# Optimization experiments

Hardware: AMD Instinct MI355X
Metric: run time of the kernel (lower is better)

The kernel has to match this reference:

```python
import jax, jax.numpy as jnp
import numpy as np
from jax import lax

N, S, F_IN = 50000, 16, 64
HID, HEADS = 128, 4
C = HID // HEADS  # 32
E = 1600000
NEG_SLOPE = 0.2


def setup_inputs() -> dict:
    key = jax.random.key(0)
    ks = jax.random.split(key, 16)
    sc = lambda *sh: 1.0 / np.sqrt(sh[-1])
    inp = {}
    inp['node_features_sequence'] = jax.random.normal(ks[0], (N, S, F_IN), dtype=jnp.float32)
    inp['edge_index'] = jax.random.randint(ks[1], (2, E), 0, N, dtype=jnp.int64)
    # GRU params (single layer, order r,z,n as in torch)
    inp['gru_w_ih'] = jax.random.normal(ks[2], (3 * HID, F_IN), jnp.float32) * sc(F_IN)
    inp['gru_w_hh'] = jax.random.normal(ks[3], (3 * HID, HID), jnp.float32) * sc(HID)
    inp['gru_b_ih'] = jax.random.normal(ks[4], (3 * HID,), jnp.float32) * 0.01
    inp['gru_b_hh'] = jax.random.normal(ks[5], (3 * HID,), jnp.float32) * 0.01
    # GAT layer 1
    inp['gat1_w'] = jax.random.normal(ks[6], (HID, HID), jnp.float32) * sc(HID)
    inp['gat1_a_src'] = jax.random.normal(ks[7], (HEADS, C), jnp.float32) * sc(C)
    inp['gat1_a_dst'] = jax.random.normal(ks[8], (HEADS, C), jnp.float32) * sc(C)
    inp['gat1_b'] = jnp.zeros((HID,), jnp.float32)
    # GAT layer 2
    inp['gat2_w'] = jax.random.normal(ks[9], (HID, HID), jnp.float32) * sc(HID)
    inp['gat2_a_src'] = jax.random.normal(ks[10], (HEADS, C), jnp.float32) * sc(C)
    inp['gat2_a_dst'] = jax.random.normal(ks[11], (HEADS, C), jnp.float32) * sc(C)
    inp['gat2_b'] = jnp.zeros((HID,), jnp.float32)
    # classifier
    inp['clf_w'] = jax.random.normal(ks[12], (1, HID), jnp.float32) * sc(HID)
    inp['clf_b'] = jnp.zeros((1,), jnp.float32)
    return inp


def gru_last(xs, w_ih, w_hh, b_ih, b_hh):
    # xs: [N, S, F] -> last hidden [N, H]
    n, _, _ = xs.shape
    h_dim = w_hh.shape[1]
    gi_all = jnp.einsum('nsf,gf->nsg', xs, w_ih) + b_ih  # [N,S,3H]
    gi_all = jnp.swapaxes(gi_all, 0, 1)  # [S,N,3H]

    def step(h, gi):
        gh = h @ w_hh.T + b_hh
        i_r, i_z, i_n = jnp.split(gi, 3, axis=-1)
        h_r, h_z, h_n = jnp.split(gh, 3, axis=-1)
        r = jax.nn.sigmoid(i_r + h_r)
        z = jax.nn.sigmoid(i_z + h_z)
        nn_ = jnp.tanh(i_n + r * h_n)
        h_new = (1.0 - z) * nn_ + z * h
        return h_new, None

    h0 = jnp.zeros((n, h_dim), xs.dtype)
    h_last, _ = lax.scan(step, h0, gi_all)
    return h_last


def gat_layer(x, src, dst, w, a_src, a_dst, b):
    # x: [N, HID]; PyG GATConv with add_self_loops, concat heads
    n = x.shape[0]
    h = (x @ w.T).reshape(n, HEADS, C)  # [N,H,C]
    a_s = jnp.einsum('nhc,hc->nh', h, a_src)  # [N,H]
    a_d = jnp.einsum('nhc,hc->nh', h, a_dst)
    e = jax.nn.leaky_relu(a_s[src] + a_d[dst], NEG_SLOPE)  # [E',H]
    m = jax.ops.segment_max(e, dst, num_segments=n)
    m = jnp.where(jnp.isfinite(m), m, 0.0)
    ex = jnp.exp(e - m[dst])
    denom = jax.ops.segment_sum(ex, dst, num_segments=n)
    alpha = ex / (denom[dst] + 1e-16)  # [E',H]
    msg = h[src] * alpha[:, :, None]  # [E',H,C]
    out = jax.ops.segment_sum(msg, dst, num_segments=n)  # [N,H,C]
    return out.reshape(n, HEADS * C) + b


def reference(node_features_sequence, edge_index,
              gru_w_ih, gru_w_hh, gru_b_ih, gru_b_hh,
              gat1_w, gat1_a_src, gat1_a_dst, gat1_b,
              gat2_w, gat2_a_src, gat2_a_dst, gat2_b,
              clf_w, clf_b):
    n = node_features_sequence.shape[0]
    # add self loops once (same structure for both layers)
    loops = jnp.arange(n, dtype=edge_index.dtype)
    src = jnp.concatenate([edge_index[0], loops])
    dst = jnp.concatenate([edge_index[1], loops])

    x = gru_last(node_features_sequence, gru_w_ih, gru_w_hh, gru_b_ih, gru_b_hh)
    x = jax.nn.elu(gat_layer(x, src, dst, gat1_w, gat1_a_src, gat1_a_dst, gat1_b))
    x = jax.nn.elu(gat_layer(x, src, dst, gat2_w, gat2_a_src, gat2_a_dst, gat2_b))
    return jax.nn.sigmoid(x @ clf_w.T + clf_b)  # [N,1]
```

## Files before the change

kernel.cpp:

```cpp
#include <hip/hip_runtime.h>
#include <hip/hip_bf16.h>
#include <hip/hip_fp16.h>
#include <math.h>

#define N_NODES 50000
#define NP      50048
#define SEQ     16
#define FIN     64
#define HID     128
#define NEDGE   1600000
#define NB_SCAN 196
#define AGG_CAP 96

typedef __attribute__((ext_vector_type(8))) short short8;
typedef __attribute__((ext_vector_type(4))) float f32x4;

__device__ __forceinline__ float lrelu02(float v) { return v > 0.f ? v : 0.2f * v; }
__device__ __forceinline__ float frcp(float v) { return __builtin_amdgcn_rcpf(v); }
__device__ __forceinline__ float ex2(float v) { return __builtin_amdgcn_exp2f(v); }
__device__ __forceinline__ float sigmoidf_(float v) { return frcp(1.f + __expf(-v)); }
__device__ __forceinline__ float eluf_(float v) { return v > 0.f ? v : (__expf(v) - 1.f); }

__device__ __forceinline__ unsigned bfpk(float lo, float hi) {
    union { __hip_bfloat162 h; unsigned u; } c;
    c.h = __float22bfloat162_rn(make_float2(lo, hi));
    return c.u;
}
__device__ __forceinline__ unsigned hfpk(float lo, float hi) {
    union { __half2 h; unsigned u; } c;
    c.h = __float22half2_rn(make_float2(lo, hi));
    return c.u;
}
__device__ __forceinline__ float2 h2f2(unsigned u) {
    union { unsigned u; __half2 h; } c;
    c.u = u;
    return __half22float2(c.h);
}
__device__ __forceinline__ short8 pack8s(float4 a, float4 b, float s) {
    union { short8 sv; unsigned u[4]; } r;
    r.u[0] = bfpk(a.x * s, a.y * s); r.u[1] = bfpk(a.z * s, a.w * s);
    r.u[2] = bfpk(b.x * s, b.y * s); r.u[3] = bfpk(b.z * s, b.w * s);
    return r.sv;
}

#define BAR() do { asm volatile("s_waitcnt lgkmcnt(0)" ::: "memory"); \
                   __builtin_amdgcn_s_barrier(); } while (0)

__global__ __launch_bounds__(512, 2) void gru_fused(
    const float* __restrict__ x,
    const float* __restrict__ w_ih,
    const float* __restrict__ w_hh,
    const float* __restrict__ b_ih,
    const float* __restrict__ b_hh,
    float* __restrict__ hout)
{
    __shared__ __align__(16) short hA[2][2][32][136];
    __shared__ __align__(16) short xB[2][2][32][72];

    const int tid  = threadIdx.x;
    const int wave = tid >> 6;
    const int lane = tid & 63;
    const int q    = lane >> 4;
    const int rl   = lane & 15;
    const int n0   = blockIdx.x * 64;
    const int ch   = wave * 16 + rl;

    const float S1 = 1.44269504088896341f;
    const float S2 = 2.88539008177792682f;
    short8 whhf[3][4];
    short8 wihf[3][2];
#pragma unroll
    for (int g = 0; g < 3; g++) {
        const float gs = (g == 2) ? S2 : S1;
        int row = g * 128 + ch;
#pragma unroll
        for (int kc = 0; kc < 4; kc++) {
            const float* p = w_hh + row * HID + kc * 32 + q * 8;
            whhf[g][kc] = pack8s(*(const float4*)p, *(const float4*)(p + 4), gs);
        }
#pragma unroll
        for (int kc = 0; kc < 2; kc++) {
            const float* p = w_ih + row * FIN + kc * 32 + q * 8;
            wihf[g][kc] = pack8s(*(const float4*)p, *(const float4*)(p + 4), gs);
        }
    }

    const float br  = (b_ih[ch] + b_hh[ch]) * S1;
    const float bz  = (b_ih[128 + ch] + b_hh[128 + ch]) * S1;
    const float bin = b_ih[256 + ch] * S2;
    const float bhn = b_hh[256 + ch] * S2;

    const int sn = tid >> 4;
    const int sk = (tid & 15) * 4;
    int g0n = n0 + sn;      if (g0n > N_NODES - 1) g0n = N_NODES - 1;
    int g1n = n0 + 32 + sn; if (g1n > N_NODES - 1) g1n = N_NODES - 1;
    const float* xs0 = x + (size_t)g0n * SEQ * FIN + sk;
    const float* xs1 = x + (size_t)g1n * SEQ * FIN + sk;

    float hreg[2][2][4];
#pragma unroll
    for (int g = 0; g < 2; g++)
#pragma unroll
        for (int mt = 0; mt < 2; mt++)
#pragma unroll
            for (int r = 0; r < 4; r++) hreg[g][mt][r] = 0.f;

    unsigned hp01[2], hp23[2];
    float4 xhold;

    {
        float4 v = *(const float4*)(xs0);
        int2 pv;
        pv.x = (int)bfpk(v.x, v.y);
        pv.y = (int)bfpk(v.z, v.w);
        *(int2*)&xB[0][0][sn][sk] = pv;
    }
    xhold = *(const float4*)(xs1);
    BAR();

#define GRU_PHASE(G, DO_HW, HWB, DO_XW, XWB, DO_XL, XLP)                          \
    {                                                                             \
        const int rb = (t - 1) & 1;                                               \
        short8 xf[2][2], hf[2][4];                                                \
        _Pragma("unroll")                                                         \
        for (int mt = 0; mt < 2; mt++)                                            \
            _Pragma("unroll")                                                     \
            for (int kc = 0; kc < 2; kc++)                                        \
                xf[mt][kc] = *(const short8*)&xB[G][t & 1][mt * 16 + rl][kc * 32 + q * 8]; \
        if (t > 0) {                                                              \
            _Pragma("unroll")                                                     \
            for (int mt = 0; mt < 2; mt++)                                        \
                _Pragma("unroll")                                                 \
                for (int kc = 0; kc < 4; kc++)                                    \
                    hf[mt][kc] = *(const short8*)&hA[G][rb][mt * 16 + rl][kc * 32 + q * 8]; \
        }                                                                         \
                         \
        if (DO_HW) {                                                              \
            _Pragma("unroll")                                                     \
            for (int mt = 0; mt < 2; mt++) {                                      \
                const int nb = mt * 16 + q * 4;                                   \
                hA[G ^ 1][HWB][nb + 0][ch] = (short)(hp01[mt] & 0xFFFF);          \
                hA[G ^ 1][HWB][nb + 1][ch] = (short)(hp01[mt] >> 16);             \
                hA[G ^ 1][HWB][nb + 2][ch] = (short)(hp23[mt] & 0xFFFF);          \
                hA[G ^ 1][HWB][nb + 3][ch] = (short)(hp23[mt] >> 16);             \
            }                                                                     \
        }                                                                         \
        if (DO_XW) {                                                              \
            int2 pv;                                                              \
            pv.x = (int)bfpk(xhold.x, xhold.y);                                   \
            pv.y = (int)bfpk(xhold.z, xhold.w);                                   \
            *(int2*)&xB[G ^ 1][XWB][sn][sk] = pv;                                 \
        }                                                                         \
        if (DO_XL) xhold = *(const float4*)(XLP);        \
        f32x4 accr[2], accz[2], accin[2], acchn[2];                               \
        _Pragma("unroll")                                                         \
        for (int mt = 0; mt < 2; mt++) {                                          \
            accr[mt] = (f32x4)0.f; accz[mt] = (f32x4)0.f;                         \
            accin[mt] = (f32x4)0.f; acchn[mt] = (f32x4)0.f;                       \
            _Pragma("unroll")                                                     \
            for (int kc = 0; kc < 2; kc++) {                                      \
                accr[mt]  = __builtin_amdgcn_mfma_f32_16x16x32_bf16(xf[mt][kc], wihf[0][kc], accr[mt], 0, 0, 0);  \
                accz[mt]  = __builtin_amdgcn_mfma_f32_16x16x32_bf16(xf[mt][kc], wihf[1][kc], accz[mt], 0, 0, 0);  \
                accin[mt] = __builtin_amdgcn_mfma_f32_16x16x32_bf16(xf[mt][kc], wihf[2][kc], accin[mt], 0, 0, 0); \
            }                                                                     \
            if (t > 0) {                                                          \
                _Pragma("unroll")                                                 \
                for (int kc = 0; kc < 4; kc++) {                                  \
                    accr[mt]  = __builtin_amdgcn_mfma_f32_16x16x32_bf16(hf[mt][kc], whhf[0][kc], accr[mt], 0, 0, 0);  \
                    accz[mt]  = __builtin_amdgcn_mfma_f32_16x16x32_bf16(hf[mt][kc], whhf[1][kc], accz[mt], 0, 0, 0);  \
                    acchn[mt] = __builtin_amdgcn_mfma_f32_16x16x32_bf16(hf[mt][kc], whhf[2][kc], acchn[mt], 0, 0, 0); \
                }                                                                 \
            }                                                                     \
        }                                                                         \
        _Pragma("unroll")                                                         \
        for (int mt = 0; mt < 2; mt++) {                                          \
            float rg[4], zg[4], et[4], hv[4];                                     \
            _Pragma("unroll")                                                     \
            for (int r = 0; r < 4; r++) {                                         \
                float er = ex2(fminf(-(accr[mt][r] + br), 60.f));                 \
                float ez = ex2(fminf(-(accz[mt][r] + bz), 60.f));                 \
                float dr = er + 1.f, dz = ez + 1.f;                               \
                float ip = frcp(dr * dz);                                         \
                rg[r] = dz * ip; zg[r] = dr * ip;                                 \
                float ap = accin[mt][r] + bin + rg[r] * (acchn[mt][r] + bhn);     \
                et[r] = ex2(fminf(ap, 120.f));                                    \
            }                                                                     \
            _Pragma("unroll")                                                     \
            for (int pr = 0; pr < 2; pr++) {                                      \
                float d0 = et[2 * pr] + 1.f, d1 = et[2 * pr + 1] + 1.f;           \
                float ipt = frcp(d0 * d1);                                        \
                float nn0 = 1.f - 2.f * (ipt * d1);                               \
                float nn1 = 1.f - 2.f * (ipt * d0);                               \
                float h0 = zg[2 * pr]     * (hreg[G][mt][2 * pr]     - nn0) + nn0; \
                float h1 = zg[2 * pr + 1] * (hreg[G][mt][2 * pr + 1] - nn1) + nn1; \
                hreg[G][mt][2 * pr] = h0; hreg[G][mt][2 * pr + 1] = h1;           \
                hv[2 * pr] = h0; hv[2 * pr + 1] = h1;                             \
            }                                                                     \
            hp01[mt] = bfpk(hv[0], hv[1]);                                        \
            hp23[mt] = bfpk(hv[2], hv[3]);                                        \
        }                                                                         \
        BAR();                                                                    \
    }

    for (int t = 0; t < SEQ; t++) {
        GRU_PHASE(0, (t > 0), ((t - 1) & 1), 1, (t & 1),
                  (t + 1 < SEQ), (xs0 + (t + 1) * FIN))
        GRU_PHASE(1, 1, (t & 1), (t + 1 < SEQ), ((t + 1) & 1),
                  (t + 1 < SEQ), (xs1 + (t + 1) * FIN))
    }
#undef GRU_PHASE

#pragma unroll
    for (int g = 0; g < 2; g++)
#pragma unroll
        for (int mt = 0; mt < 2; mt++)
#pragma unroll
            for (int r = 0; r < 4; r++)
                hout[(size_t)(n0 + g * 32 + mt * 16 + q * 4 + r) * HID + ch] = hreg[g][mt][r];
}

__global__ void prep_weights(const float* __restrict__ g1w, const float* __restrict__ g2w,
                             float* __restrict__ g1T, float* __restrict__ g2T)
{
    int i = blockIdx.x * 256 + threadIdx.x;
    if (i < 128 * 128) {
        int k = i >> 7, g = i & 127;
        g1T[i] = g1w[g * 128 + k];
        g2T[i] = g2w[g * 128 + k];
    }
}

__global__ void count_edges(const int* __restrict__ dst, int* __restrict__ deg, int e)
{
    int i = blockIdx.x * 256 + threadIdx.x;
    if (i < e) atomicAdd(&deg[dst[i]], 1);
}

__device__ __forceinline__ int block_scan_inc(int v)
{
    int tid = threadIdx.x, lane = tid & 63, w = tid >> 6;
#pragma unroll
    for (int off = 1; off < 64; off <<= 1) {
        int tmp = __shfl_up(v, off, 64);
        if (lane >= off) v += tmp;
    }
    __shared__ int wsum[4];
    if (lane == 63) wsum[w] = v;
    __syncthreads();
    int add = 0;
    for (int i = 0; i < w; i++) add += wsum[i];
    return v + add;
}

__global__ void scan_block_sums(const int* __restrict__ deg, int* __restrict__ bsum, int n)
{
    int i = blockIdx.x * 256 + threadIdx.x;
    int v = (i < n) ? deg[i] : 0;
#pragma unroll
    for (int off = 32; off >= 1; off >>= 1) v += __shfl_xor(v, off, 64);
    __shared__ int ws[4];
    if ((threadIdx.x & 63) == 0) ws[threadIdx.x >> 6] = v;
    __syncthreads();
    if (threadIdx.x == 0) bsum[blockIdx.x] = ws[0] + ws[1] + ws[2] + ws[3];
}

__global__ void scan_bsum(int* __restrict__ bsum, int nb)
{
    int tid = threadIdx.x;
    int v = (tid < nb) ? bsum[tid] : 0;
    v = block_scan_inc(v);
    if (tid < nb) bsum[tid] = v;
}

__global__ void scan_final(const int* __restrict__ deg, const int* __restrict__ bsum,
                           int* __restrict__ rp, int n)
{
    int i = blockIdx.x * 256 + threadIdx.x;
    int v = (i < n) ? deg[i] : 0;
    int s = block_scan_inc(v);
    int add = (blockIdx.x > 0) ? bsum[blockIdx.x - 1] : 0;
    if (i < n) rp[i + 1] = s + add;
    if (i == 0) rp[0] = 0;
}

__global__ void fill_edges(const int* __restrict__ src, const int* __restrict__ dst,
                           const int* __restrict__ rp, int* __restrict__ cur,
                           int* __restrict__ col, int e)
{
    int i = blockIdx.x * 256 + threadIdx.x;
    if (i < e) {
        int d = dst[i];
        int pos = atomicAdd(&cur[d], 1);
        col[rp[d] + pos] = src[i];
    }
}

__global__ __launch_bounds__(256) void proj_attn(
    const float* __restrict__ x, const float* __restrict__ wT,
    const float* __restrict__ a_src, const float* __restrict__ a_dst,
    unsigned* __restrict__ hph, float* __restrict__ as_, float* __restrict__ ad_)
{
    __shared__ float xt[32][33];
    __shared__ float wt[32][128];
    __shared__ float ot[32][132];
    const int tid = threadIdx.x;
    const int tx = tid & 7;
    const int ty = tid >> 3;
    const int n0 = blockIdx.x * 32;
    float acc[4][4];
#pragma unroll
    for (int i = 0; i < 4; i++)
#pragma unroll
        for (int j = 0; j < 4; j++) acc[i][j] = 0.f;

    for (int k0 = 0; k0 < 128; k0 += 32) {
        __syncthreads();
#pragma unroll
        for (int i = 0; i < 4; i++) {
            int flat = tid + i * 256;
            int n = flat >> 5, k = flat & 31;
            xt[n][k] = x[(n0 + n) * HID + k0 + k];
        }
#pragma unroll
        for (int i = 0; i < 16; i++) {
            int flat = tid + i * 256;
            int kk = flat >> 7, g = flat & 127;
            wt[kk][g] = wT[(k0 + kk) * HID + g];
        }
        __syncthreads();
#pragma unroll 8
        for (int kk = 0; kk < 32; kk++) {
            float xv[4];
#pragma unroll
            for (int i = 0; i < 4; i++) xv[i] = xt[tx * 4 + i][kk];
            float4 wv = *(const float4*)&wt[kk][ty * 4];
#pragma unroll
            for (int i = 0; i < 4; i++) {
                acc[i][0] = fmaf(xv[i], wv.x, acc[i][0]);
                acc[i][1] = fmaf(xv[i], wv.y, acc[i][1]);
                acc[i][2] = fmaf(xv[i], wv.z, acc[i][2]);
                acc[i][3] = fmaf(xv[i], wv.w, acc[i][3]);
            }
        }
    }
#pragma unroll
    for (int i = 0; i < 4; i++) {
        int node = tx * 4 + i;
        ot[node][ty * 4 + 0] = acc[i][0];
        ot[node][ty * 4 + 1] = acc[i][1];
        ot[node][ty * 4 + 2] = acc[i][2];
        ot[node][ty * 4 + 3] = acc[i][3];
        uint2 pv;
        pv.x = hfpk(acc[i][0], acc[i][1]);
        pv.y = hfpk(acc[i][2], acc[i][3]);
        *(uint2*)&hph[(size_t)(n0 + node) * 64 + ty * 2] = pv;
    }
    __syncthreads();
    if (tid < 128) {
        int node = tid >> 2, head = tid & 3;
        const float* ar = a_src + head * 32;
        const float* br = a_dst + head * 32;
        float s = 0.f, d = 0.f;
#pragma unroll
        for (int j = 0; j < 32; j += 4) {
            float4 hv = *(const float4*)&ot[node][head * 32 + j];
            float4 av = *(const float4*)&ar[j];
            float4 bv = *(const float4*)&br[j];
            s += hv.x * av.x + hv.y * av.y + hv.z * av.z + hv.w * av.w;
            d += hv.x * bv.x + hv.y * bv.y + hv.z * bv.z + hv.w * bv.w;
        }
        as_[(n0 + node) * 4 + head] = s;
        ad_[(n0 + node) * 4 + head] = d;
    }
}

template <bool CLF>
__global__ __launch_bounds__(256) void gat_agg(
    const unsigned* __restrict__ hph, const float* __restrict__ as_,
    const float* __restrict__ ad_, const int* __restrict__ rp,
    const int* __restrict__ col, const float* __restrict__ bias,
    float* __restrict__ out, const float* __restrict__ cw,
    const float* __restrict__ cb, int n_nodes)
{
    __shared__ float exl[4][AGG_CAP][4];
    const int widx = threadIdx.x >> 6;
    const int lane = threadIdx.x & 63;
    const int n = blockIdx.x * 4 + widx;
    if (n >= n_nodes) return;

    const int e0 = rp[n], e1 = rp[n + 1];
    const int deg = e1 - e0;
    float4 adv = *(const float4*)&ad_[n * 4];
    float4 asn = *(const float4*)&as_[n * 4];
    float xs0 = __expf(lrelu02(asn.x + adv.x)), xs1 = __expf(lrelu02(asn.y + adv.y));
    float xs2 = __expf(lrelu02(asn.z + adv.z)), xs3 = __expf(lrelu02(asn.w + adv.w));

    float d0 = 0.f, d1 = 0.f, d2 = 0.f, d3 = 0.f;
    for (int e = e0 + lane; e < e1; e += 64) {
        int s = col[e];
        float4 a = *(const float4*)&as_[s * 4];
        float x0 = __expf(lrelu02(a.x + adv.x));
        float x1 = __expf(lrelu02(a.y + adv.y));
        float x2 = __expf(lrelu02(a.z + adv.z));
        float x3 = __expf(lrelu02(a.w + adv.w));
        int idx = e - e0;
        if (idx < AGG_CAP) {
            exl[widx][idx][0] = x0; exl[widx][idx][1] = x1;
            exl[widx][idx][2] = x2; exl[widx][idx][3] = x3;
        }
        d0 += x0; d1 += x1; d2 += x2; d3 += x3;
    }
#pragma unroll
    for (int off = 32; off >= 1; off >>= 1) {
        d0 += __shfl_xor(d0, off, 64);
        d1 += __shfl_xor(d1, off, 64);
        d2 += __shfl_xor(d2, off, 64);
        d3 += __shfl_xor(d3, off, 64);
    }
    d0 += xs0; d1 += xs1; d2 += xs2; d3 += xs3;
    float i0 = frcp(d0 + 1e-16f), i1 = frcp(d1 + 1e-16f);
    float i2 = frcp(d2 + 1e-16f), i3 = frcp(d3 + 1e-16f);

    const int head = lane >> 4;
    float invh = (head == 0) ? i0 : (head == 1) ? i1 : (head == 2) ? i2 : i3;
    float exsh = (head == 0) ? xs0 : (head == 1) ? xs1 : (head == 2) ? xs2 : xs3;
    float adh  = (head == 0) ? adv.x : (head == 1) ? adv.y : (head == 2) ? adv.z : adv.w;

    float2 sv = h2f2(hph[(size_t)n * 64 + lane]);
    float acc0 = exsh * sv.x;
    float acc1 = exsh * sv.y;

    if (deg <= AGG_CAP) {
        int e = e0;
        for (; e + 4 <= e1; e += 4) {
            int s_[4]; float w_[4]; unsigned u_[4];
#pragma unroll
            for (int u = 0; u < 4; u++) {
                s_[u] = col[e + u];
                w_[u] = exl[widx][e + u - e0][head];
            }
#pragma unroll
            for (int u = 0; u < 4; u++)
                u_[u] = hph[(size_t)s_[u] * 64 + lane];
#pragma unroll
            for (int u = 0; u < 4; u++) {
                float2 f = h2f2(u_[u]);
                acc0 = fmaf(w_[u], f.x, acc0);
                acc1 = fmaf(w_[u], f.y, acc1);
            }
        }
        for (; e < e1; e++) {
            int s = col[e];
            float w = exl[widx][e - e0][head];
            float2 f = h2f2(hph[(size_t)s * 64 + lane]);
            acc0 = fmaf(w, f.x, acc0);
            acc1 = fmaf(w, f.y, acc1);
        }
    } else {
        for (int e = e0; e < e1; e++) {
            int s = col[e];
            int idx = e - e0;
            float w;
            if (idx < AGG_CAP) w = exl[widx][idx][head];
            else               w = __expf(lrelu02(as_[s * 4 + head] + adh));
            float2 f = h2f2(hph[(size_t)s * 64 + lane]);
            acc0 = fmaf(w, f.x, acc0);
            acc1 = fmaf(w, f.y, acc1);
        }
    }

    float2 b2 = *(const float2*)&bias[2 * lane];
    float o0 = eluf_(acc0 * invh + b2.x);
    float o1 = eluf_(acc1 * invh + b2.y);
    if (CLF) {
        float2 cwv = *(const float2*)&cw[2 * lane];
        float v = o0 * cwv.x + o1 * cwv.y;
#pragma unroll
        for (int off = 32; off >= 1; off >>= 1) v += __shfl_xor(v, off, 64);
        if (lane == 0) out[n] = sigmoidf_(v + cb[0]);
    } else {
        *(float2*)&out[(size_t)n * HID + 2 * lane] = make_float2(o0, o1);
    }
}

extern "C" void kernel_launch(void* const* d_in, const int* in_sizes, int n_in,
                              void* d_out, int out_size, void* d_ws, size_t ws_size,
                              hipStream_t stream)
{
    const float* x     = (const float*)d_in[0];
    const int*   ei    = (const int*)d_in[1];
    const float* w_ih  = (const float*)d_in[2];
    const float* w_hh  = (const float*)d_in[3];
    const float* b_ih  = (const float*)d_in[4];
    const float* b_hh  = (const float*)d_in[5];
    const float* g1w   = (const float*)d_in[6];
    const float* g1as  = (const float*)d_in[7];
    const float* g1ad  = (const float*)d_in[8];
    const float* g1b   = (const float*)d_in[9];
    const float* g2w   = (const float*)d_in[10];
    const float* g2as  = (const float*)d_in[11];
    const float* g2ad  = (const float*)d_in[12];
    const float* g2b   = (const float*)d_in[13];
    const float* cw    = (const float*)d_in[14];
    const float* cb    = (const float*)d_in[15];
    float* out = (float*)d_out;

    char* wsb = (char*)d_ws;
    size_t off = 0;
    auto alc = [&](size_t bytes) { size_t o = off; off += (bytes + 255) & ~(size_t)255; return o; };

    float*    bufA = (float*)(wsb + alc((size_t)NP * HID * 4));
    float*    bufC = (float*)(wsb + alc((size_t)NP * HID * 4));
    unsigned* hph  = (unsigned*)(wsb + alc((size_t)NP * 64 * 4));
    float*    as_  = (float*)(wsb + alc((size_t)NP * 4 * 4));
    float*    ad_  = (float*)(wsb + alc((size_t)NP * 4 * 4));
    float*    g1T  = (float*)(wsb + alc((size_t)128 * 128 * 4));
    float*    g2T  = (float*)(wsb + alc((size_t)128 * 128 * 4));
    int*      rp   = (int*)(wsb + alc((size_t)(N_NODES + 1) * 4));
    int*      deg  = (int*)(wsb + alc((size_t)N_NODES * 4));
    int*      cur  = (int*)(wsb + alc((size_t)N_NODES * 4));
    int*      col  = (int*)(wsb + alc((size_t)NEDGE * 4));
    int*      bsum = (int*)(wsb + alc((size_t)256 * 4));

    const int* src = ei;
    const int* dst = ei + NEDGE;

    hipMemsetAsync(deg, 0, (size_t)N_NODES * 4, stream);
    hipMemsetAsync(cur, 0, (size_t)N_NODES * 4, stream);

    prep_weights<<<64, 256, 0, stream>>>(g1w, g2w, g1T, g2T);

    count_edges<<<NEDGE / 256, 256, 0, stream>>>(dst, deg, NEDGE);
    scan_block_sums<<<NB_SCAN, 256, 0, stream>>>(deg, bsum, N_NODES);
    scan_bsum<<<1, 256, 0, stream>>>(bsum, NB_SCAN);
    scan_final<<<NB_SCAN, 256, 0, stream>>>(deg, bsum, rp, N_NODES);
    fill_edges<<<NEDGE / 256, 256, 0, stream>>>(src, dst, rp, cur, col, NEDGE);

    gru_fused<<<NP / 64, 512, 0, stream>>>(x, w_ih, w_hh, b_ih, b_hh, bufA);

    proj_attn<<<NP / 32, 256, 0, stream>>>(bufA, g1T, g1as, g1ad, hph, as_, ad_);
    gat_agg<false><<<(N_NODES + 3) / 4, 256, 0, stream>>>(hph, as_, ad_, rp, col, g1b, bufC,
                                                          nullptr, nullptr, N_NODES);

    proj_attn<<<NP / 32, 256, 0, stream>>>(bufC, g2T, g2as, g2ad, hph, as_, ad_);
    gat_agg<true><<<(N_NODES + 3) / 4, 256, 0, stream>>>(hph, as_, ad_, rp, col, g2b, out,
                                                         cw, cb, N_NODES);
}
```

Before: 840.8 us.

## Software-pipeline GRU gate math of one group behind MFMA of the other

Restructures the two-group GRU recurrence so each phase issues the MFMAs for group G and then runs the sigmoid/tanh gate math for the other group's accumulators from the previous phase. Accumulators are kept across phases in registers, and the hidden-state write to LDS moves into the deferred gate block. The aim is to overlap transcendental VALU work with matrix-core work between barriers. In exchange it holds more live accumulator registers, which may lower occupancy, and needs a trailing gate block after the loop.

```diff
diff --git a/kernel.cpp b/kernel.cpp
--- a/kernel.cpp
+++ b/kernel.cpp
@@ -105,8 +105,8 @@
 #pragma unroll
             for (int r = 0; r < 4; r++) hreg[g][mt][r] = 0.f;
 
-    unsigned hp01[2], hp23[2];
-    float4 xhold;
+    f32x4 accr[2][2], accz[2][2], accin[2][2], acchn[2][2];
+    float4 xh[2];
 
     {
         float4 v = *(const float4*)(xs0);
@@ -115,12 +115,48 @@
         pv.y = (int)bfpk(v.z, v.w);
         *(int2*)&xB[0][0][sn][sk] = pv;
     }
-    xhold = *(const float4*)(xs1);
+    xh[1] = *(const float4*)(xs1);
     BAR();
 
-#define GRU_PHASE(G, DO_HW, HWB, DO_XW, XWB, DO_XL, XLP)                          \
+#define GATE_BLOCK(B, PG, DO_HW, HWB)                                             \
     {                                                                             \
-        const int rb = (t - 1) & 1;                                               \
+        _Pragma("unroll")                                                         \
+        for (int mt = 0; mt < 2; mt++) {                                          \
+            float rg[4], zg[4], et[4];                                            \
+            _Pragma("unroll")                                                     \
+            for (int r = 0; r < 4; r++) {                                         \
+                float er  = ex2(fminf(-(accr[B][mt][r] + br), 60.f));             \
+                float ezv = ex2(fminf(-(accz[B][mt][r] + bz), 60.f));             \
+                float dr = er + 1.f, dz = ezv + 1.f;                              \
+                float ip = frcp(dr * dz);                                         \
+                rg[r] = dz * ip; zg[r] = dr * ip;                                 \
+                float ap = accin[B][mt][r] + bin + rg[r] * (acchn[B][mt][r] + bhn); \
+                et[r] = ex2(fminf(ap, 120.f));                                    \
+            }                                                                     \
+            _Pragma("unroll")                                                     \
+            for (int pr = 0; pr < 2; pr++) {                                      \
+                float dd0 = et[2 * pr] + 1.f, dd1 = et[2 * pr + 1] + 1.f;         \
+                float ipt = frcp(dd0 * dd1);                                      \
+                float nn0 = 1.f - 2.f * (ipt * dd1);                              \
+                float nn1 = 1.f - 2.f * (ipt * dd0);                              \
+                float h0 = zg[2 * pr]     * (hreg[PG][mt][2 * pr]     - nn0) + nn0; \
+                float h1 = zg[2 * pr + 1] * (hreg[PG][mt][2 * pr + 1] - nn1) + nn1; \
+                hreg[PG][mt][2 * pr] = h0; hreg[PG][mt][2 * pr + 1] = h1;         \
+            }                                                                     \
+            if (DO_HW) {                                                          \
+                unsigned u01 = bfpk(hreg[PG][mt][0], hreg[PG][mt][1]);            \
+                unsigned u23 = bfpk(hreg[PG][mt][2], hreg[PG][mt][3]);            \
+                const int nb = mt * 16 + q * 4;                                   \
+                hA[PG][HWB][nb + 0][ch] = (short)(u01 & 0xFFFF);                  \
+                hA[PG][HWB][nb + 1][ch] = (short)(u01 >> 16);                     \
+                hA[PG][HWB][nb + 2][ch] = (short)(u23 & 0xFFFF);                  \
+                hA[PG][HWB][nb + 3][ch] = (short)(u23 >> 16);                     \
+            }                                                                     \
+        }                                                                         \
+    }
+
+#define GRU_PHASE(G, PG, DO_GATE, HWB, DO_HW, DO_XW, XWB, XPTR)                   \
+    {                                                                             \
         short8 xf[2][2], hf[2][4];                                                \
         _Pragma("unroll")                                                         \
         for (int mt = 0; mt < 2; mt++)                                            \
@@ -132,83 +168,49 @@
             for (int mt = 0; mt < 2; mt++)                                        \
                 _Pragma("unroll")                                                 \
                 for (int kc = 0; kc < 4; kc++)                                    \
-                    hf[mt][kc] = *(const short8*)&hA[G][rb][mt * 16 + rl][kc * 32 + q * 8]; \
+                    hf[mt][kc] = *(const short8*)&hA[G][(t - 1) & 1][mt * 16 + rl][kc * 32 + q * 8]; \
         }                                                                         \
-                         \
-        if (DO_HW) {                                                              \
-            _Pragma("unroll")                                                     \
-            for (int mt = 0; mt < 2; mt++) {                                      \
-                const int nb = mt * 16 + q * 4;                                   \
-                hA[G ^ 1][HWB][nb + 0][ch] = (short)(hp01[mt] & 0xFFFF);          \
-                hA[G ^ 1][HWB][nb + 1][ch] = (short)(hp01[mt] >> 16);             \
-                hA[G ^ 1][HWB][nb + 2][ch] = (short)(hp23[mt] & 0xFFFF);          \
-                hA[G ^ 1][HWB][nb + 3][ch] = (short)(hp23[mt] >> 16);             \
+        if (t + 1 < SEQ) xh[G] = *(const float4*)(XPTR + (t + 1) * FIN);          \
+        _Pragma("unroll")                                                         \
+        for (int mt = 0; mt < 2; mt++) {                                          \
+            accr[G][mt]  = __builtin_amdgcn_mfma_f32_16x16x32_bf16(xf[mt][0], wihf[0][0], (f32x4)0.f, 0, 0, 0); \
+            accz[G][mt]  = __builtin_amdgcn_mfma_f32_16x16x32_bf16(xf[mt][0], wihf[1][0], (f32x4)0.f, 0, 0, 0); \
+            accin[G][mt] = __builtin_amdgcn_mfma_f32_16x16x32_bf16(xf[mt][0], wihf[2][0], (f32x4)0.f, 0, 0, 0); \
+            accr[G][mt]  = __builtin_amdgcn_mfma_f32_16x16x32_bf16(xf[mt][1], wihf[0][1], accr[G][mt], 0, 0, 0); \
+            accz[G][mt]  = __builtin_amdgcn_mfma_f32_16x16x32_bf16(xf[mt][1], wihf[1][1], accz[G][mt], 0, 0, 0); \
+            accin[G][mt] = __builtin_amdgcn_mfma_f32_16x16x32_bf16(xf[mt][1], wihf[2][1], accin[G][mt], 0, 0, 0); \
+            if (t > 0) {                                                          \
+                acchn[G][mt] = __builtin_amdgcn_mfma_f32_16x16x32_bf16(hf[mt][0], whhf[2][0], (f32x4)0.f, 0, 0, 0); \
+                _Pragma("unroll")                                                 \
+                for (int kc = 0; kc < 4; kc++) {                                  \
+                    accr[G][mt]  = __builtin_amdgcn_mfma_f32_16x16x32_bf16(hf[mt][kc], whhf[0][kc], accr[G][mt], 0, 0, 0);  \
+                    accz[G][mt]  = __builtin_amdgcn_mfma_f32_16x16x32_bf16(hf[mt][kc], whhf[1][kc], accz[G][mt], 0, 0, 0);  \
+                }                                                                 \
+                _Pragma("unroll")                                                 \
+                for (int kc = 1; kc < 4; kc++)                                    \
+                    acchn[G][mt] = __builtin_amdgcn_mfma_f32_16x16x32_bf16(hf[mt][kc], whhf[2][kc], acchn[G][mt], 0, 0, 0); \
+            } else {                                                              \
+                acchn[G][mt] = (f32x4)0.f;                                        \
             }                                                                     \
         }                                                                         \
+        if (DO_GATE) GATE_BLOCK(PG, PG, DO_HW, HWB);                              \
         if (DO_XW) {                                                              \
             int2 pv;                                                              \
-            pv.x = (int)bfpk(xhold.x, xhold.y);                                   \
-            pv.y = (int)bfpk(xhold.z, xhold.w);                                   \
-            *(int2*)&xB[G ^ 1][XWB][sn][sk] = pv;                                 \
-        }                                                                         \
-        if (DO_XL) xhold = *(const float4*)(XLP);        \
-        f32x4 accr[2], accz[2], accin[2], acchn[2];                               \
-        _Pragma("unroll")                                                         \
-        for (int mt = 0; mt < 2; mt++) {                                          \
-            accr[mt] = (f32x4)0.f; accz[mt] = (f32x4)0.f;                         \
-            accin[mt] = (f32x4)0.f; acchn[mt] = (f32x4)0.f;                       \
-            _Pragma("unroll")                                                     \
-            for (int kc = 0; kc < 2; kc++) {                                      \
-                accr[mt]  = __builtin_amdgcn_mfma_f32_16x16x32_bf16(xf[mt][kc], wihf[0][kc], accr[mt], 0, 0, 0);  \
-                accz[mt]  = __builtin_amdgcn_mfma_f32_16x16x32_bf16(xf[mt][kc], wihf[1][kc], accz[mt], 0, 0, 0);  \
-                accin[mt] = __builtin_amdgcn_mfma_f32_16x16x32_bf16(xf[mt][kc], wihf[2][kc], accin[mt], 0, 0, 0); \
-            }                                                                     \
-            if (t > 0) {                                                          \
-                _Pragma("unroll")                                                 \
-                for (int kc = 0; kc < 4; kc++) {                                  \
-                    accr[mt]  = __builtin_amdgcn_mfma_f32_16x16x32_bf16(hf[mt][kc], whhf[0][kc], accr[mt], 0, 0, 0);  \
-                    accz[mt]  = __builtin_amdgcn_mfma_f32_16x16x32_bf16(hf[mt][kc], whhf[1][kc], accz[mt], 0, 0, 0);  \
-                    acchn[mt] = __builtin_amdgcn_mfma_f32_16x16x32_bf16(hf[mt][kc], whhf[2][kc], acchn[mt], 0, 0, 0); \
-                }                                                                 \
-            }                                                                     \
-        }                                                                         \
-        _Pragma("unroll")                                                         \
-        for (int mt = 0; mt < 2; mt++) {                                          \
-            float rg[4], zg[4], et[4], hv[4];                                     \
-            _Pragma("unroll")                                                     \
-            for (int r = 0; r < 4; r++) {                                         \
-                float er = ex2(fminf(-(accr[mt][r] + br), 60.f));                 \
-                float ez = ex2(fminf(-(accz[mt][r] + bz), 60.f));                 \
-                float dr = er + 1.f, dz = ez + 1.f;                               \
-                float ip = frcp(dr * dz);                                         \
-                rg[r] = dz * ip; zg[r] = dr * ip;                                 \
-                float ap = accin[mt][r] + bin + rg[r] * (acchn[mt][r] + bhn);     \
-                et[r] = ex2(fminf(ap, 120.f));                                    \
-            }                                                                     \
-            _Pragma("unroll")                                                     \
-            for (int pr = 0; pr < 2; pr++) {                                      \
-                float d0 = et[2 * pr] + 1.f, d1 = et[2 * pr + 1] + 1.f;           \
-                float ipt = frcp(d0 * d1);                                        \
-                float nn0 = 1.f - 2.f * (ipt * d1);                               \
-                float nn1 = 1.f - 2.f * (ipt * d0);                               \
-                float h0 = zg[2 * pr]     * (hreg[G][mt][2 * pr]     - nn0) + nn0; \
-                float h1 = zg[2 * pr + 1] * (hreg[G][mt][2 * pr + 1] - nn1) + nn1; \
-                hreg[G][mt][2 * pr] = h0; hreg[G][mt][2 * pr + 1] = h1;           \
-                hv[2 * pr] = h0; hv[2 * pr + 1] = h1;                             \
-            }                                                                     \
-            hp01[mt] = bfpk(hv[0], hv[1]);                                        \
-            hp23[mt] = bfpk(hv[2], hv[3]);                                        \
+            pv.x = (int)bfpk(xh[PG].x, xh[PG].y);                                 \
+            pv.y = (int)bfpk(xh[PG].z, xh[PG].w);                                 \
+            *(int2*)&xB[PG][XWB][sn][sk] = pv;                                    \
         }                                                                         \
         BAR();                                                                    \
     }
 
     for (int t = 0; t < SEQ; t++) {
-        GRU_PHASE(0, (t > 0), ((t - 1) & 1), 1, (t & 1),
-                  (t + 1 < SEQ), (xs0 + (t + 1) * FIN))
-        GRU_PHASE(1, 1, (t & 1), (t + 1 < SEQ), ((t + 1) & 1),
-                  (t + 1 < SEQ), (xs1 + (t + 1) * FIN))
+        GRU_PHASE(0, 1, (t > 0), ((t - 1) & 1), (t > 0), 1, (t & 1), xs0)
+        GRU_PHASE(1, 0, 1, (t & 1), (t + 1 < SEQ), (t + 1 < SEQ), ((t + 1) & 1), xs1)
     }
 #undef GRU_PHASE
+
+    GATE_BLOCK(1, 1, 0, 0);
+#undef GATE_BLOCK
 
 #pragma unroll
     for (int g = 0; g < 2; g++)
```

Result: no change. 828.5 us (-1.5%).
